# Kernel tuning notes

Hardware: AMD Instinct MI355X
Metric: run time of the kernel (lower is better)

Reference implementation:

```python
import jax, jax.numpy as jnp
import numpy as np

B, T, DM = 2, 512, 1024
H, DH = 16, 64          # n_heads, d_head = d_model // n_heads
D, R = 32, 4            # d_manifold, metric_net rank
TEMP_MIN = 0.5


def _rope_tables(t_len, d_head):
    inv_freq = 1.0 / (10000.0 ** (jnp.arange(0, d_head, 2, dtype=jnp.float32) / d_head))
    t = jnp.arange(t_len, dtype=jnp.float32)
    freqs = t[:, None] * inv_freq[None, :]          # [T, d_head//2]
    emb = jnp.concatenate([freqs, freqs], axis=-1)  # [T, d_head]
    return jnp.cos(emb), jnp.sin(emb)


def _apply_rope(x, cos, sin):
    # x: [B, H, T, d_head]
    half = x.shape[-1] // 2
    x1, x2 = x[..., :half], x[..., half:]
    c1 = cos[None, None, :, :half]
    s1 = sin[None, None, :, :half]
    return jnp.concatenate([x1 * c1 - x2 * s1, x1 * s1 + x2 * c1], axis=-1)


def setup_inputs() -> dict:
    key = jax.random.key(0)
    ks = jax.random.split(key, 9)
    s = 0.02
    return {
        "x": jax.random.normal(ks[0], (B, T, DM), dtype=jnp.float32),
        "Wq": s * jax.random.normal(ks[1], (DM, DM), dtype=jnp.float32),
        "Wk": s * jax.random.normal(ks[2], (DM, DM), dtype=jnp.float32),
        "Wv": s * jax.random.normal(ks[3], (DM, DM), dtype=jnp.float32),
        "Wo": s * jax.random.normal(ks[4], (DM, DM), dtype=jnp.float32),
        "Wqm": s * jax.random.normal(ks[5], (DH, D), dtype=jnp.float32),
        "Wkm": s * jax.random.normal(ks[6], (DH, D), dtype=jnp.float32),
        "Wmetric": s * jax.random.normal(ks[7], (D, D * R), dtype=jnp.float32),
        "temperature": jnp.asarray(1.0, dtype=jnp.float32),
    }


def reference(x, Wq, Wk, Wv, Wo, Wqm, Wkm, Wmetric, temperature):
    b, t, c = x.shape
    # projections -> [B, H, T, d_head]
    def split_heads(y):
        return y.reshape(b, t, H, DH).transpose(0, 2, 1, 3)
    q = split_heads(x @ Wq)
    k = split_heads(x @ Wk)
    v = split_heads(x @ Wv)

    cos, sin = _rope_tables(t, DH)
    q = _apply_rope(q, cos, sin)
    k = _apply_rope(k, cos, sin)

    # manifold coordinates in (0,1): [B, H, T, D]
    qm = jax.nn.sigmoid(jnp.einsum('bhtd,dm->bhtm', q, Wqm))
    km = jax.nn.sigmoid(jnp.einsum('bhtd,dm->bhtm', k, Wkm))

    # low-rank metric factor U(q): [B, H, T, D, R]
    U = jnp.einsum('bhtm,mn->bhtn', qm, Wmetric).reshape(b, H, t, D, R)

    # Euclidean part: ||q_i - k_j||^2 = |q|^2 + |k|^2 - 2 q.k  -> [B,H,T,T]
    q2 = jnp.sum(qm * qm, axis=-1)
    k2 = jnp.sum(km * km, axis=-1)
    qk = jnp.einsum('bhid,bhjd->bhij', qm, km)
    dist_euc = q2[..., :, None] + k2[..., None, :] - 2.0 * qk

    # low-rank part: ||U_i^T (q_i - k_j)||^2, factorized as U_i^T q_i - U_i^T k_j
    Uq = jnp.einsum('bhidr,bhid->bhir', U, qm)          # [B,H,T,R]
    Uk = jnp.einsum('bhidr,bhjd->bhijr', U, km)         # [B,H,T,T,R]
    dist_lr = jnp.sum((Uq[:, :, :, None, :] - Uk) ** 2, axis=-1)

    dist_sq = jnp.maximum(dist_euc + dist_lr, 0.0)

    temp = jnp.maximum(temperature, TEMP_MIN)
    attn = -dist_sq / temp

    causal = jnp.triu(jnp.ones((t, t), dtype=bool), k=1)
    attn = jnp.where(causal[None, None], -jnp.inf, attn)
    attn = jax.nn.softmax(attn, axis=-1)

    out = jnp.einsum('bhij,bhjd->bhid', attn, v)        # [B,H,T,d_head]
    out = out.transpose(0, 2, 1, 3).reshape(b, t, c)
    return out @ Wo
```

## Files before the change

### kernel.cpp

```cpp
#include <hip/hip_runtime.h>
#include <cmath>

constexpr int B_  = 2;
constexpr int T_  = 512;
constexpr int DM_ = 1024;
constexpr int H_  = 16;
constexpr int DH_ = 64;
constexpr int D_  = 32;
constexpr int R_  = 4;
constexpr int BH_ = B_ * H_;

typedef __bf16 bf16x8 __attribute__((ext_vector_type(8)));
typedef float  f32x4  __attribute__((ext_vector_type(4)));
typedef unsigned short u16x8 __attribute__((ext_vector_type(8)));

__device__ __forceinline__ unsigned short f2bf(float f) {
    unsigned u = __float_as_uint(f);
    return (unsigned short)((u + 0x7fffu + ((u >> 16) & 1u)) >> 16);
}
__device__ __forceinline__ float bf2f(unsigned short v) {
    return __uint_as_float((unsigned)v << 16);
}

__device__ __forceinline__ void gload16(const void* g, void* l) {
    __builtin_amdgcn_global_load_lds(
        (const __attribute__((address_space(1))) void*)g,
        (__attribute__((address_space(3))) void*)l, 16, 0, 0);
}

__global__ __launch_bounds__(256) void prep_kernel(
    const float* __restrict__ x,
    const float* __restrict__ Wq, const float* __restrict__ Wk,
    const float* __restrict__ Wv, const float* __restrict__ Wo,
    unsigned short* __restrict__ xb,
    unsigned short* __restrict__ wqb, unsigned short* __restrict__ wkb,
    unsigned short* __restrict__ wvb, unsigned short* __restrict__ wob)
{
    const int t = threadIdx.x;
    const int z = blockIdx.z;
    if (z == 4) {
        int base = (blockIdx.y * 16 + blockIdx.x) * 4096 + t * 16;
#pragma unroll
        for (int c = 0; c < 4; ++c) {
            float4 v = *(const float4*)&x[base + c * 4];
            ushort4 o = { f2bf(v.x), f2bf(v.y), f2bf(v.z), f2bf(v.w) };
            *(ushort4*)&xb[base + c * 4] = o;
        }
        return;
    }
    __shared__ __align__(16) unsigned short Ls[64][72];
    const float* W = (z == 0) ? Wq : (z == 1) ? Wk : (z == 2) ? Wv : Wo;
    unsigned short* O = (z == 0) ? wqb : (z == 1) ? wkb : (z == 2) ? wvb : wob;
    const int k0 = blockIdx.x * 64;
    const int n0 = blockIdx.y * 64;
#pragma unroll
    for (int it = 0; it < 4; ++it) {
        int r = it * 16 + (t >> 4);
        int c = (t & 15) * 4;
        float4 v4 = *(const float4*)&W[(size_t)(k0 + r) * DM_ + n0 + c];
        Ls[c + 0][r] = f2bf(v4.x); Ls[c + 1][r] = f2bf(v4.y);
        Ls[c + 2][r] = f2bf(v4.z); Ls[c + 3][r] = f2bf(v4.w);
    }
    __syncthreads();
#pragma unroll
    for (int it = 0; it < 2; ++it) {
        int nl = it * 32 + (t >> 3);
        int kc = (t & 7) * 8;
        *(u16x8*)&O[(size_t)(n0 + nl) * DM_ + k0 + kc] = *(const u16x8*)&Ls[nl][kc];
    }
}

template <int EPI>
__global__ __launch_bounds__(256) void mfma_gemm64(
    const unsigned short* __restrict__ A,
    const unsigned short* __restrict__ Bt0,
    const unsigned short* __restrict__ Bt1,
    const unsigned short* __restrict__ Bt2,
    float* __restrict__ C0, float* __restrict__ C1,
    unsigned short* __restrict__ vT)
{
    __shared__ __align__(16) unsigned short As[64 * 32];
    __shared__ __align__(16) unsigned short Bs[64 * 32];
    const int tid  = threadIdx.x;
    const int lane = tid & 63;
    const int w    = tid >> 6;
    const int wm   = (w & 1) * 32;
    const int wn   = (w >> 1) * 32;

    const int bm = blockIdx.y * 64;
    int bn, which = 0;
    const unsigned short* Bt;
    if (EPI == 0) {
        int n0 = blockIdx.x * 64;
        which = n0 >> 10;
        bn = n0 & 1023;
        Bt = (which == 0) ? Bt0 : (which == 1) ? Bt1 : Bt2;
    } else {
        bn = blockIdx.x * 64;
        Bt = Bt0;
    }

    f32x4 acc[2][2] = {};
    const int sr = tid >> 2;
    const int sc = (tid & 3) * 8;
    const unsigned short* Ap = A  + (size_t)(bm + sr) * DM_ + sc;
    const unsigned short* Bp = Bt + (size_t)(bn + sr) * DM_ + sc;
    unsigned short* AsP = &As[sr * 32 + sc];
    unsigned short* BsP = &Bs[sr * 32 + sc];
    const int fr = lane & 15;
    const int fq = (lane >> 4) * 8;

    for (int k0 = 0; k0 < DM_; k0 += 32) {
        gload16(Ap + k0, AsP);
        gload16(Bp + k0, BsP);
        __syncthreads();
        bf16x8 af[2], bfr[2];
#pragma unroll
        for (int i = 0; i < 2; ++i) {
            af[i]  = *(const bf16x8*)&As[(wm + i * 16 + fr) * 32 + fq];
            bfr[i] = *(const bf16x8*)&Bs[(wn + i * 16 + fr) * 32 + fq];
        }
#pragma unroll
        for (int mi = 0; mi < 2; ++mi)
#pragma unroll
            for (int ni = 0; ni < 2; ++ni)
                acc[mi][ni] = __builtin_amdgcn_mfma_f32_16x16x32_bf16(
                    af[mi], bfr[ni], acc[mi][ni], 0, 0, 0);
        __syncthreads();
    }

#pragma unroll
    for (int mi = 0; mi < 2; ++mi)
#pragma unroll
        for (int ni = 0; ni < 2; ++ni) {
            f32x4 a = acc[mi][ni];
            int col = bn + wn + ni * 16 + (lane & 15);
#pragma unroll
            for (int r = 0; r < 4; ++r) {
                int row = bm + wm + mi * 16 + (lane >> 4) * 4 + r;
                if (EPI == 0) {
                    int h = col >> 6, d = col & 63;
                    int bb = row >> 9, tt = row & (T_ - 1);
                    if (which == 2) {
                        vT[(((size_t)bb * H_ + h) * DH_ + d) * T_ + tt] = f2bf(a[r]);
                    } else {
                        float* C = (which == 0) ? C0 : C1;
                        C[(((size_t)bb * H_ + h) * T_ + tt) * DH_ + d] = a[r];
                    }
                } else {
                    C0[(size_t)row * DM_ + col] = a[r];
                }
            }
        }
}

__global__ __launch_bounds__(256) void feat_both(
    const float* __restrict__ q_raw, const float* __restrict__ k_raw,
    const float* __restrict__ Wqm,   const float* __restrict__ Wkm,
    const float* __restrict__ Wmetric,
    unsigned short* __restrict__ a_hi, unsigned short* __restrict__ a_lo,
    unsigned short* __restrict__ km_hi, unsigned short* __restrict__ km_lo,
    float* __restrict__ q2p, float* __restrict__ k2,
    unsigned short* __restrict__ Urb)
{
    const bool QSIDE = (blockIdx.y == 0);
    const float* raw = QSIDE ? q_raw : k_raw;
    const float* Wm  = QSIDE ? Wqm   : Wkm;

    __shared__ float qrs[4][64];
    __shared__ float qms[4][32];
    __shared__ float Us[4][128];
    __shared__ float Uqs[4][4];
    const int tid  = threadIdx.x;
    const int w    = tid >> 6;
    const int lane = tid & 63;
    const int row  = blockIdx.x * 4 + w;
    const int t    = row & (T_ - 1);
    const int bh   = row >> 9;

    float rv = raw[(size_t)row * 64 + lane];
    int   fi = lane & 31;
    float ang = (float)t * expf((float)fi * -0.28782313662425575f);
    float s, c;
    sincosf(ang, &s, &c);
    float partner = __shfl_xor(rv, 32);
    float qr = (lane < 32) ? (rv * c - partner * s) : (partner * s + rv * c);
    qrs[w][lane] = qr;
    __syncthreads();

    if (lane < 32) {
        float acc = 0.f;
#pragma unroll 8
        for (int d = 0; d < 64; ++d) acc += qrs[w][d] * Wm[d * 32 + lane];
        qms[w][lane] = 1.0f / (1.0f + __expf(-acc));
    }
    __syncthreads();

    if (QSIDE) {
        float a0 = 0.f, a1 = 0.f;
#pragma unroll 8
        for (int m = 0; m < 32; ++m) {
            float qv = qms[w][m];
            a0 += qv * Wmetric[m * 128 + lane];
            a1 += qv * Wmetric[m * 128 + 64 + lane];
        }
        Us[w][lane] = a0; Us[w][64 + lane] = a1;
        {
            int r0 = lane & 3, d0 = lane >> 2;
            int d1 = 16 + (lane >> 2);
            Urb[(((size_t)bh * R_ + r0) * T_ + t) * D_ + d0] = f2bf(a0);
            Urb[(((size_t)bh * R_ + r0) * T_ + t) * D_ + d1] = f2bf(a1);
        }
        __syncthreads();
        if (lane < 4) {
            float acc = 0.f;
#pragma unroll
            for (int d = 0; d < 32; ++d) acc += Us[w][d * 4 + lane] * qms[w][d];
            Uqs[w][lane] = acc;
        }
        __syncthreads();
        if (lane < 32) {
            float b = Uqs[w][0] * Us[w][lane * 4 + 0]
                    + Uqs[w][1] * Us[w][lane * 4 + 1]
                    + Uqs[w][2] * Us[w][lane * 4 + 2]
                    + Uqs[w][3] * Us[w][lane * 4 + 3];
            float a = qms[w][lane] + b;
            unsigned short hi = f2bf(a);
            unsigned short lo = f2bf(a - bf2f(hi));
            size_t off = (size_t)row * 32 + lane;
            a_hi[off] = hi; a_lo[off] = lo;
        }
        if (lane == 0) {
            float acc = 0.f;
#pragma unroll
            for (int m = 0; m < 32; ++m) acc += qms[w][m] * qms[w][m];
#pragma unroll
            for (int r = 0; r < 4; ++r) acc += Uqs[w][r] * Uqs[w][r];
            q2p[row] = acc;
        }
    } else {
        if (lane < 32) {
            float v = qms[w][lane];
            unsigned short hi = f2bf(v);
            unsigned short lo = f2bf(v - bf2f(hi));
            size_t off = (size_t)row * 32 + lane;
            km_hi[off] = hi; km_lo[off] = lo;
        }
        if (lane == 0) {
            float acc = 0.f;
#pragma unroll
            for (int m = 0; m < 32; ++m) acc += qms[w][m] * qms[w][m];
            k2[row] = acc;
        }
    }
}

constexpr int PROW = 40;
__global__ __launch_bounds__(256) void attn_mfma(
    const unsigned short* __restrict__ a_hi, const unsigned short* __restrict__ a_lo,
    const unsigned short* __restrict__ km_hi, const unsigned short* __restrict__ km_lo,
    const unsigned short* __restrict__ Urb,
    const float* __restrict__ q2p, const float* __restrict__ k2,
    const float* __restrict__ temp_p, const unsigned short* __restrict__ vT,
    unsigned short* __restrict__ ctxb)
{
    __shared__ __align__(16) unsigned short P_lds[4][32 * PROW];
    __shared__ __align__(16) float OP[4][32][64];
    __shared__ float ML[4][32];

    const int itile = blockIdx.x, bh = blockIdx.y;
    const int i0 = itile * 32;
    const int tid = threadIdx.x, w = tid >> 6, lane = tid & 63;
    const int l15 = lane & 15, quad = lane >> 4;

    const float inv_temp = 1.0f / fmaxf(temp_p[0], 0.5f);

    bf16x8 Ahi[2], Alo[2], Aur[4][2];
#pragma unroll
    for (int mi = 0; mi < 2; ++mi) {
        size_t ab = ((size_t)bh * T_ + i0 + mi * 16 + l15) * 32 + quad * 8;
        Ahi[mi] = *(const bf16x8*)&a_hi[ab];
        Alo[mi] = *(const bf16x8*)&a_lo[ab];
#pragma unroll
        for (int r = 0; r < 4; ++r)
            Aur[r][mi] = *(const bf16x8*)
                &Urb[(((size_t)bh * R_ + r) * T_ + i0 + mi * 16 + l15) * 32 + quad * 8];
    }
    float q2r[2][4];
#pragma unroll
    for (int mi = 0; mi < 2; ++mi)
#pragma unroll
        for (int rg = 0; rg < 4; ++rg)
            q2r[mi][rg] = q2p[(size_t)bh * T_ + i0 + mi * 16 + quad * 4 + rg];

    f32x4 Oacc[2][4] = {};
    float psum[2][4] = {};

    for (int jt = w; jt <= itile; jt += 4) {
        const int j0 = jt * 32;
        bf16x8 Bhi[2], Blo[2];
#pragma unroll
        for (int ni = 0; ni < 2; ++ni) {
            size_t kb = ((size_t)bh * T_ + j0 + ni * 16 + l15) * 32 + quad * 8;
            Bhi[ni] = *(const bf16x8*)&km_hi[kb];
            Blo[ni] = *(const bf16x8*)&km_lo[kb];
        }
        f32x4 acc[2][2] = {};
#pragma unroll
        for (int mi = 0; mi < 2; ++mi)
#pragma unroll
            for (int ni = 0; ni < 2; ++ni) {
                acc[mi][ni] = __builtin_amdgcn_mfma_f32_16x16x32_bf16(
                    Alo[mi], Bhi[ni], acc[mi][ni], 0, 0, 0);
                acc[mi][ni] = __builtin_amdgcn_mfma_f32_16x16x32_bf16(
                    Ahi[mi], Blo[ni], acc[mi][ni], 0, 0, 0);
                acc[mi][ni] = __builtin_amdgcn_mfma_f32_16x16x32_bf16(
                    Ahi[mi], Bhi[ni], acc[mi][ni], 0, 0, 0);
            }
        f32x4 sq[2][2] = {};
#pragma unroll
        for (int r = 0; r < 4; ++r) {
            f32x4 ar[2][2] = {};
#pragma unroll
            for (int mi = 0; mi < 2; ++mi)
#pragma unroll
                for (int ni = 0; ni < 2; ++ni)
                    ar[mi][ni] = __builtin_amdgcn_mfma_f32_16x16x32_bf16(
                        Aur[r][mi], Bhi[ni], ar[mi][ni], 0, 0, 0);
#pragma unroll
            for (int mi = 0; mi < 2; ++mi)
#pragma unroll
                for (int ni = 0; ni < 2; ++ni)
                    sq[mi][ni] += ar[mi][ni] * ar[mi][ni];
        }
        float k2c[2];
#pragma unroll
        for (int ni = 0; ni < 2; ++ni)
            k2c[ni] = k2[(size_t)bh * T_ + j0 + ni * 16 + l15];
        const bool diag = (jt == itile);
#pragma unroll
        for (int mi = 0; mi < 2; ++mi)
#pragma unroll
            for (int ni = 0; ni < 2; ++ni)
#pragma unroll
                for (int rg = 0; rg < 4; ++rg) {
                    float dist = q2r[mi][rg] + k2c[ni]
                               - 2.f * acc[mi][ni][rg] + sq[mi][ni][rg];
                    float sc = -fmaxf(dist, 0.f) * inv_temp;
                    if (diag && (ni * 16 + l15) > (mi * 16 + quad * 4 + rg))
                        sc = -1e30f;
                    float p = __expf(sc);
                    psum[mi][rg] += p;
                    P_lds[w][(mi * 16 + quad * 4 + rg) * PROW + ni * 16 + l15] = f2bf(p);
                }
        bf16x8 Pf[2], Vf[4];
#pragma unroll
        for (int mi = 0; mi < 2; ++mi)
            Pf[mi] = *(const bf16x8*)&P_lds[w][(mi * 16 + l15) * PROW + quad * 8];
#pragma unroll
        for (int n4 = 0; n4 < 4; ++n4)
            Vf[n4] = *(const bf16x8*)
                &vT[((size_t)bh * DH_ + n4 * 16 + l15) * T_ + j0 + quad * 8];
#pragma unroll
        for (int mi = 0; mi < 2; ++mi)
#pragma unroll
            for (int n4 = 0; n4 < 4; ++n4)
                Oacc[mi][n4] = __builtin_amdgcn_mfma_f32_16x16x32_bf16(
                    Pf[mi], Vf[n4], Oacc[mi][n4], 0, 0, 0);
    }

#pragma unroll
    for (int mi = 0; mi < 2; ++mi)
#pragma unroll
        for (int rg = 0; rg < 4; ++rg) {
            float v = psum[mi][rg];
            v += __shfl_xor(v, 1); v += __shfl_xor(v, 2);
            v += __shfl_xor(v, 4); v += __shfl_xor(v, 8);
            psum[mi][rg] = v;
        }
    if (l15 == 0)
#pragma unroll
        for (int mi = 0; mi < 2; ++mi)
#pragma unroll
            for (int rg = 0; rg < 4; ++rg)
                ML[w][mi * 16 + quad * 4 + rg] = psum[mi][rg];
#pragma unroll
    for (int mi = 0; mi < 2; ++mi)
#pragma unroll
        for (int n4 = 0; n4 < 4; ++n4)
#pragma unroll
            for (int rg = 0; rg < 4; ++rg)
                OP[w][mi * 16 + quad * 4 + rg][n4 * 16 + l15] = Oacc[mi][n4][rg];
    __syncthreads();

    const int ii = tid >> 3, ds = tid & 7;
    float l = ML[0][ii] + ML[1][ii] + ML[2][ii] + ML[3][ii];
    float O[8] = {};
#pragma unroll
    for (int wv = 0; wv < 4; ++wv) {
        float4 o0 = *(const float4*)&OP[wv][ii][ds * 8];
        float4 o1 = *(const float4*)&OP[wv][ii][ds * 8 + 4];
        O[0] += o0.x; O[1] += o0.y; O[2] += o0.z; O[3] += o0.w;
        O[4] += o1.x; O[5] += o1.y; O[6] += o1.z; O[7] += o1.w;
    }
    const float inv = 1.0f / l;
    const int b = bh >> 4, h = bh & 15;
    u16x8 o;
#pragma unroll
    for (int dd = 0; dd < 8; ++dd) o[dd] = f2bf(O[dd] * inv);
    *(u16x8*)&ctxb[((size_t)b * T_ + i0 + ii) * DM_ + h * 64 + ds * 8] = o;
}

extern "C" void kernel_launch(void* const* d_in, const int* in_sizes, int n_in,
                              void* d_out, int out_size, void* d_ws, size_t ws_size,
                              hipStream_t stream)
{
    const float* x       = (const float*)d_in[0];
    const float* Wq      = (const float*)d_in[1];
    const float* Wk      = (const float*)d_in[2];
    const float* Wv      = (const float*)d_in[3];
    const float* Wo      = (const float*)d_in[4];
    const float* Wqm     = (const float*)d_in[5];
    const float* Wkm     = (const float*)d_in[6];
    const float* Wmetric = (const float*)d_in[7];
    const float* temp    = (const float*)d_in[8];
    float* out = (float*)d_out;
    float* ws  = (float*)d_ws;

    float* q_raw = ws;
    float* k_raw = q_raw + (size_t)BH_ * T_ * DH_;
    float* q2p   = k_raw + (size_t)BH_ * T_ * DH_;
    float* k2    = q2p   + (size_t)BH_ * T_;
    unsigned short* xb    = (unsigned short*)(k2 + (size_t)BH_ * T_);
    unsigned short* wqb   = xb    + (size_t)DM_ * DM_;
    unsigned short* wkb   = wqb   + (size_t)DM_ * DM_;
    unsigned short* wvb   = wkb   + (size_t)DM_ * DM_;
    unsigned short* wob   = wvb   + (size_t)DM_ * DM_;
    unsigned short* a_hi  = wob   + (size_t)DM_ * DM_;
    unsigned short* a_lo  = a_hi  + (size_t)BH_ * T_ * D_;
    unsigned short* kmhi  = a_lo  + (size_t)BH_ * T_ * D_;
    unsigned short* kmlo  = kmhi  + (size_t)BH_ * T_ * D_;
    unsigned short* Urb   = kmlo  + (size_t)BH_ * T_ * D_;
    unsigned short* vT    = Urb   + (size_t)BH_ * R_ * T_ * D_;
    unsigned short* ctxb  = (unsigned short*)q_raw;

    prep_kernel<<<dim3(16, 16, 5), 256, 0, stream>>>(
        x, Wq, Wk, Wv, Wo, xb, wqb, wkb, wvb, wob);
    mfma_gemm64<0><<<dim3(48, 16), 256, 0, stream>>>(
        xb, wqb, wkb, wvb, q_raw, k_raw, vT);
    feat_both<<<dim3(BH_ * T_ / 4, 2), 256, 0, stream>>>(
        q_raw, k_raw, Wqm, Wkm, Wmetric,
        a_hi, a_lo, kmhi, kmlo, q2p, k2, Urb);
    attn_mfma<<<dim3(T_ / 32, BH_), 256, 0, stream>>>(
        a_hi, a_lo, kmhi, kmlo, Urb, q2p, k2, temp, vT, ctxb);
    mfma_gemm64<1><<<dim3(16, 16), 256, 0, stream>>>(
        ctxb, wob, nullptr, nullptr, out, nullptr, nullptr);
}
```

Before: 156.2 us.

## Fuse RoPE and manifold feature computation into QKV GEMM epilogue

```diff
diff --git a/kernel.cpp b/kernel.cpp
--- a/kernel.cpp
+++ b/kernel.cpp
@@ -70,14 +70,194 @@
     }
 }
 
-template <int EPI>
-__global__ __launch_bounds__(256) void mfma_gemm64(
+__global__ __launch_bounds__(256) void qkv_feat_gemm(
     const unsigned short* __restrict__ A,
-    const unsigned short* __restrict__ Bt0,
-    const unsigned short* __restrict__ Bt1,
-    const unsigned short* __restrict__ Bt2,
-    float* __restrict__ C0, float* __restrict__ C1,
-    unsigned short* __restrict__ vT)
+    const unsigned short* __restrict__ wqb, const unsigned short* __restrict__ wkb,
+    const unsigned short* __restrict__ wvb,
+    const float* __restrict__ Wqm, const float* __restrict__ Wkm,
+    const float* __restrict__ Wmetric,
+    unsigned short* __restrict__ a_hi, unsigned short* __restrict__ a_lo,
+    unsigned short* __restrict__ km_hi, unsigned short* __restrict__ km_lo,
+    float* __restrict__ q2p, float* __restrict__ k2,
+    unsigned short* __restrict__ Urb, unsigned short* __restrict__ vT)
+{
+    __shared__ union {
+        struct { __align__(16) unsigned short As[64 * 32];
+                 __align__(16) unsigned short Bs[64 * 32]; } g;
+        struct { float Ct[64][65]; float qm[64][33]; } f;
+    } sh;
+
+    const int tid  = threadIdx.x;
+    const int lane = tid & 63;
+    const int w    = tid >> 6;
+    const int wm   = (w & 1) * 32;
+    const int wn   = (w >> 1) * 32;
+    const int l15  = lane & 15, quad = lane >> 4;
+
+    const int bm = blockIdx.y * 64;
+    const int n0 = blockIdx.x * 64;
+    const int which = n0 >> 10;
+    const int bn = n0 & 1023;
+    const int h  = bn >> 6;
+    const unsigned short* Bt = (which == 0) ? wqb : (which == 1) ? wkb : wvb;
+
+    f32x4 acc[2][2] = {};
+    const int sr = tid >> 2;
+    const int sc = (tid & 3) * 8;
+    const unsigned short* Ap = A  + (size_t)(bm + sr) * DM_ + sc;
+    const unsigned short* Bp = Bt + (size_t)(bn + sr) * DM_ + sc;
+    unsigned short* AsP = &sh.g.As[sr * 32 + sc];
+    unsigned short* BsP = &sh.g.Bs[sr * 32 + sc];
+
+    for (int k0 = 0; k0 < DM_; k0 += 32) {
+        gload16(Ap + k0, AsP);
+        gload16(Bp + k0, BsP);
+        __syncthreads();
+        bf16x8 af[2], bfr[2];
+#pragma unroll
+        for (int i = 0; i < 2; ++i) {
+            af[i]  = *(const bf16x8*)&sh.g.As[(wm + i * 16 + l15) * 32 + quad * 8];
+            bfr[i] = *(const bf16x8*)&sh.g.Bs[(wn + i * 16 + l15) * 32 + quad * 8];
+        }
+#pragma unroll
+        for (int mi = 0; mi < 2; ++mi)
+#pragma unroll
+            for (int ni = 0; ni < 2; ++ni)
+                acc[mi][ni] = __builtin_amdgcn_mfma_f32_16x16x32_bf16(
+                    af[mi], bfr[ni], acc[mi][ni], 0, 0, 0);
+        __syncthreads();
+    }
+
+    if (which == 2) {
+#pragma unroll
+        for (int mi = 0; mi < 2; ++mi)
+#pragma unroll
+            for (int ni = 0; ni < 2; ++ni) {
+                f32x4 a = acc[mi][ni];
+                int d = wn + ni * 16 + l15;
+#pragma unroll
+                for (int r = 0; r < 4; ++r) {
+                    int m = bm + wm + mi * 16 + quad * 4 + r;
+                    int bb = m >> 9, tt = m & (T_ - 1);
+                    vT[(((size_t)bb * H_ + h) * DH_ + d) * T_ + tt] = f2bf(a[r]);
+                }
+            }
+        return;
+    }
+
+#pragma unroll
+    for (int mi = 0; mi < 2; ++mi)
+#pragma unroll
+        for (int ni = 0; ni < 2; ++ni) {
+            f32x4 a = acc[mi][ni];
+            int cl = wn + ni * 16 + l15;
+#pragma unroll
+            for (int r = 0; r < 4; ++r)
+                sh.f.Ct[wm + mi * 16 + quad * 4 + r][cl] = a[r];
+        }
+    __syncthreads();
+
+    for (int e = tid; e < 2048; e += 256) {
+        int row = e >> 5, d = e & 31;
+        int t = (bm + row) & (T_ - 1);
+        float ang = (float)t * expf((float)d * -0.28782313662425575f);
+        float s, c;
+        sincosf(ang, &s, &c);
+        float v1 = sh.f.Ct[row][d], v2 = sh.f.Ct[row][d + 32];
+        sh.f.Ct[row][d]      = v1 * c - v2 * s;
+        sh.f.Ct[row][d + 32] = v1 * s + v2 * c;
+    }
+    __syncthreads();
+
+    const float* Wm = (which == 0) ? Wqm : Wkm;
+    const int r  = tid >> 2, c = tid & 3, mg = c * 8;
+    float a8[8] = {};
+    for (int d = 0; d < 64; ++d) {
+        float qr = sh.f.Ct[r][d];
+        float4 w0 = *(const float4*)&Wm[d * 32 + mg];
+        float4 w1 = *(const float4*)&Wm[d * 32 + mg + 4];
+        a8[0] = fmaf(qr, w0.x, a8[0]); a8[1] = fmaf(qr, w0.y, a8[1]);
+        a8[2] = fmaf(qr, w0.z, a8[2]); a8[3] = fmaf(qr, w0.w, a8[3]);
+        a8[4] = fmaf(qr, w1.x, a8[4]); a8[5] = fmaf(qr, w1.y, a8[5]);
+        a8[6] = fmaf(qr, w1.z, a8[6]); a8[7] = fmaf(qr, w1.w, a8[7]);
+    }
+#pragma unroll
+    for (int j = 0; j < 8; ++j) a8[j] = 1.0f / (1.0f + __expf(-a8[j]));
+
+    const int m_ = bm + r;
+    const int b_ = m_ >> 9, t_ = m_ & (T_ - 1);
+    const int bh = b_ * H_ + h;
+    const size_t rowg = (size_t)bh * T_ + t_;
+
+    if (which == 1) {
+        u16x8 hi8, lo8;
+#pragma unroll
+        for (int j = 0; j < 8; ++j) {
+            unsigned short hv = f2bf(a8[j]);
+            hi8[j] = hv; lo8[j] = f2bf(a8[j] - bf2f(hv));
+        }
+        *(u16x8*)&km_hi[rowg * 32 + mg] = hi8;
+        *(u16x8*)&km_lo[rowg * 32 + mg] = lo8;
+        float p = 0.f;
+#pragma unroll
+        for (int j = 0; j < 8; ++j) p = fmaf(a8[j], a8[j], p);
+        p += __shfl_xor(p, 1); p += __shfl_xor(p, 2);
+        if (c == 0) k2[rowg] = p;
+        return;
+    }
+
+#pragma unroll
+    for (int j = 0; j < 8; ++j) sh.f.qm[r][mg + j] = a8[j];
+    __syncthreads();
+
+    const int nc = c * 32;
+    float U[32] = {};
+    for (int m = 0; m < 32; ++m) {
+        float qv = sh.f.qm[r][m];
+        const float* wrow = &Wmetric[m * 128 + nc];
+#pragma unroll
+        for (int n4 = 0; n4 < 8; ++n4) {
+            float4 wv = *(const float4*)&wrow[n4 * 4];
+            U[n4 * 4 + 0] = fmaf(qv, wv.x, U[n4 * 4 + 0]);
+            U[n4 * 4 + 1] = fmaf(qv, wv.y, U[n4 * 4 + 1]);
+            U[n4 * 4 + 2] = fmaf(qv, wv.z, U[n4 * 4 + 2]);
+            U[n4 * 4 + 3] = fmaf(qv, wv.w, U[n4 * 4 + 3]);
+        }
+    }
+    float uq[4] = {};
+#pragma unroll
+    for (int n = 0; n < 32; ++n) {
+        int nn = nc + n, d = nn >> 2, rr = nn & 3;
+        Urb[((size_t)(bh * R_ + rr) * T_ + t_) * D_ + d] = f2bf(U[n]);
+        uq[rr] = fmaf(U[n], sh.f.qm[r][d], uq[rr]);
+    }
+#pragma unroll
+    for (int rr = 0; rr < 4; ++rr) {
+        uq[rr] += __shfl_xor(uq[rr], 1);
+        uq[rr] += __shfl_xor(uq[rr], 2);
+    }
+    u16x8 hi8, lo8;
+    float p = 0.f;
+#pragma unroll
+    for (int j = 0; j < 8; ++j) {
+        float qmv = sh.f.qm[r][mg + j];
+        float av = qmv + uq[0] * U[j * 4 + 0] + uq[1] * U[j * 4 + 1]
+                       + uq[2] * U[j * 4 + 2] + uq[3] * U[j * 4 + 3];
+        unsigned short hv = f2bf(av);
+        hi8[j] = hv; lo8[j] = f2bf(av - bf2f(hv));
+        p = fmaf(qmv, qmv, p);
+    }
+    *(u16x8*)&a_hi[rowg * 32 + mg] = hi8;
+    *(u16x8*)&a_lo[rowg * 32 + mg] = lo8;
+    p += __shfl_xor(p, 1); p += __shfl_xor(p, 2);
+    if (c == 0)
+        q2p[rowg] = p + uq[0] * uq[0] + uq[1] * uq[1]
+                      + uq[2] * uq[2] + uq[3] * uq[3];
+}
+
+__global__ __launch_bounds__(256) void out_gemm64(
+    const unsigned short* __restrict__ A, const unsigned short* __restrict__ Bt,
+    float* __restrict__ C)
 {
     __shared__ __align__(16) unsigned short As[64 * 32];
     __shared__ __align__(16) unsigned short Bs[64 * 32];
@@ -86,19 +266,8 @@
     const int w    = tid >> 6;
     const int wm   = (w & 1) * 32;
     const int wn   = (w >> 1) * 32;
-
     const int bm = blockIdx.y * 64;
-    int bn, which = 0;
-    const unsigned short* Bt;
-    if (EPI == 0) {
-        int n0 = blockIdx.x * 64;
-        which = n0 >> 10;
-        bn = n0 & 1023;
-        Bt = (which == 0) ? Bt0 : (which == 1) ? Bt1 : Bt2;
-    } else {
-        bn = blockIdx.x * 64;
-        Bt = Bt0;
-    }
+    const int bn = blockIdx.x * 64;
 
     f32x4 acc[2][2] = {};
     const int sr = tid >> 2;
@@ -128,7 +297,6 @@
                     af[mi], bfr[ni], acc[mi][ni], 0, 0, 0);
         __syncthreads();
     }
-
 #pragma unroll
     for (int mi = 0; mi < 2; ++mi)
 #pragma unroll
@@ -138,121 +306,9 @@
 #pragma unroll
             for (int r = 0; r < 4; ++r) {
                 int row = bm + wm + mi * 16 + (lane >> 4) * 4 + r;
-                if (EPI == 0) {
-                    int h = col >> 6, d = col & 63;
-                    int bb = row >> 9, tt = row & (T_ - 1);
-                    if (which == 2) {
-                        vT[(((size_t)bb * H_ + h) * DH_ + d) * T_ + tt] = f2bf(a[r]);
-                    } else {
-                        float* C = (which == 0) ? C0 : C1;
-                        C[(((size_t)bb * H_ + h) * T_ + tt) * DH_ + d] = a[r];
-                    }
-                } else {
-                    C0[(size_t)row * DM_ + col] = a[r];
-                }
+                C[(size_t)row * DM_ + col] = a[r];
             }
         }
-}
-
-__global__ __launch_bounds__(256) void feat_both(
-    const float* __restrict__ q_raw, const float* __restrict__ k_raw,
-    const float* __restrict__ Wqm,   const float* __restrict__ Wkm,
-    const float* __restrict__ Wmetric,
-    unsigned short* __restrict__ a_hi, unsigned short* __restrict__ a_lo,
-    unsigned short* __restrict__ km_hi, unsigned short* __restrict__ km_lo,
-    float* __restrict__ q2p, float* __restrict__ k2,
-    unsigned short* __restrict__ Urb)
-{
-    const bool QSIDE = (blockIdx.y == 0);
-    const float* raw = QSIDE ? q_raw : k_raw;
-    const float* Wm  = QSIDE ? Wqm   : Wkm;
-
-    __shared__ float qrs[4][64];
-    __shared__ float qms[4][32];
-    __shared__ float Us[4][128];
-    __shared__ float Uqs[4][4];
-    const int tid  = threadIdx.x;
-    const int w    = tid >> 6;
-    const int lane = tid & 63;
-    const int row  = blockIdx.x * 4 + w;
-    const int t    = row & (T_ - 1);
-    const int bh   = row >> 9;
-
-    float rv = raw[(size_t)row * 64 + lane];
-    int   fi = lane & 31;
-    float ang = (float)t * expf((float)fi * -0.28782313662425575f);
-    float s, c;
-    sincosf(ang, &s, &c);
-    float partner = __shfl_xor(rv, 32);
-    float qr = (lane < 32) ? (rv * c - partner * s) : (partner * s + rv * c);
-    qrs[w][lane] = qr;
-    __syncthreads();
-
-    if (lane < 32) {
-        float acc = 0.f;
-#pragma unroll 8
-        for (int d = 0; d < 64; ++d) acc += qrs[w][d] * Wm[d * 32 + lane];
-        qms[w][lane] = 1.0f / (1.0f + __expf(-acc));
-    }
-    __syncthreads();
-
-    if (QSIDE) {
-        float a0 = 0.f, a1 = 0.f;
-#pragma unroll 8
-        for (int m = 0; m < 32; ++m) {
-            float qv = qms[w][m];
-            a0 += qv * Wmetric[m * 128 + lane];
-            a1 += qv * Wmetric[m * 128 + 64 + lane];
-        }
-        Us[w][lane] = a0; Us[w][64 + lane] = a1;
-        {
-            int r0 = lane & 3, d0 = lane >> 2;
-            int d1 = 16 + (lane >> 2);
-            Urb[(((size_t)bh * R_ + r0) * T_ + t) * D_ + d0] = f2bf(a0);
-            Urb[(((size_t)bh * R_ + r0) * T_ + t) * D_ + d1] = f2bf(a1);
-        }
-        __syncthreads();
-        if (lane < 4) {
-            float acc = 0.f;
-#pragma unroll
-            for (int d = 0; d < 32; ++d) acc += Us[w][d * 4 + lane] * qms[w][d];
-            Uqs[w][lane] = acc;
-        }
-        __syncthreads();
-        if (lane < 32) {
-            float b = Uqs[w][0] * Us[w][lane * 4 + 0]
-                    + Uqs[w][1] * Us[w][lane * 4 + 1]
-                    + Uqs[w][2] * Us[w][lane * 4 + 2]
-                    + Uqs[w][3] * Us[w][lane * 4 + 3];
-            float a = qms[w][lane] + b;
-            unsigned short hi = f2bf(a);
-            unsigned short lo = f2bf(a - bf2f(hi));
-            size_t off = (size_t)row * 32 + lane;
-            a_hi[off] = hi; a_lo[off] = lo;
-        }
-        if (lane == 0) {
-            float acc = 0.f;
-#pragma unroll
-            for (int m = 0; m < 32; ++m) acc += qms[w][m] * qms[w][m];
-#pragma unroll
-            for (int r = 0; r < 4; ++r) acc += Uqs[w][r] * Uqs[w][r];
-            q2p[row] = acc;
-        }
-    } else {
-        if (lane < 32) {
-            float v = qms[w][lane];
-            unsigned short hi = f2bf(v);
-            unsigned short lo = f2bf(v - bf2f(hi));
-            size_t off = (size_t)row * 32 + lane;
-            km_hi[off] = hi; km_lo[off] = lo;
-        }
-        if (lane == 0) {
-            float acc = 0.f;
-#pragma unroll
-            for (int m = 0; m < 32; ++m) acc += qms[w][m] * qms[w][m];
-            k2[row] = acc;
-        }
-    }
 }
 
 constexpr int PROW = 40;
@@ -427,32 +483,27 @@
     float* out = (float*)d_out;
     float* ws  = (float*)d_ws;
 
-    float* q_raw = ws;
-    float* k_raw = q_raw + (size_t)BH_ * T_ * DH_;
-    float* q2p   = k_raw + (size_t)BH_ * T_ * DH_;
-    float* k2    = q2p   + (size_t)BH_ * T_;
-    unsigned short* xb    = (unsigned short*)(k2 + (size_t)BH_ * T_);
-    unsigned short* wqb   = xb    + (size_t)DM_ * DM_;
-    unsigned short* wkb   = wqb   + (size_t)DM_ * DM_;
-    unsigned short* wvb   = wkb   + (size_t)DM_ * DM_;
-    unsigned short* wob   = wvb   + (size_t)DM_ * DM_;
-    unsigned short* a_hi  = wob   + (size_t)DM_ * DM_;
-    unsigned short* a_lo  = a_hi  + (size_t)BH_ * T_ * D_;
-    unsigned short* kmhi  = a_lo  + (size_t)BH_ * T_ * D_;
-    unsigned short* kmlo  = kmhi  + (size_t)BH_ * T_ * D_;
-    unsigned short* Urb   = kmlo  + (size_t)BH_ * T_ * D_;
-    unsigned short* vT    = Urb   + (size_t)BH_ * R_ * T_ * D_;
-    unsigned short* ctxb  = (unsigned short*)q_raw;
+    float* q2p = ws;
+    float* k2  = q2p + (size_t)BH_ * T_;
+    unsigned short* xb   = (unsigned short*)(k2 + (size_t)BH_ * T_);
+    unsigned short* wqb  = xb   + (size_t)DM_ * DM_;
+    unsigned short* wkb  = wqb  + (size_t)DM_ * DM_;
+    unsigned short* wvb  = wkb  + (size_t)DM_ * DM_;
+    unsigned short* wob  = wvb  + (size_t)DM_ * DM_;
+    unsigned short* a_hi = wob  + (size_t)DM_ * DM_;
+    unsigned short* a_lo = a_hi + (size_t)BH_ * T_ * D_;
+    unsigned short* kmhi = a_lo + (size_t)BH_ * T_ * D_;
+    unsigned short* kmlo = kmhi + (size_t)BH_ * T_ * D_;
+    unsigned short* Urb  = kmlo + (size_t)BH_ * T_ * D_;
+    unsigned short* vT   = Urb  + (size_t)BH_ * R_ * T_ * D_;
+    unsigned short* ctxb = vT   + (size_t)BH_ * DH_ * T_;
 
     prep_kernel<<<dim3(16, 16, 5), 256, 0, stream>>>(
         x, Wq, Wk, Wv, Wo, xb, wqb, wkb, wvb, wob);
-    mfma_gemm64<0><<<dim3(48, 16), 256, 0, stream>>>(
-        xb, wqb, wkb, wvb, q_raw, k_raw, vT);
-    feat_both<<<dim3(BH_ * T_ / 4, 2), 256, 0, stream>>>(
-        q_raw, k_raw, Wqm, Wkm, Wmetric,
-        a_hi, a_lo, kmhi, kmlo, q2p, k2, Urb);
+    qkv_feat_gemm<<<dim3(48, 16), 256, 0, stream>>>(
+        xb, wqb, wkb, wvb, Wqm, Wkm, Wmetric,
+        a_hi, a_lo, kmhi, kmlo, q2p, k2, Urb, vT);
     attn_mfma<<<dim3(T_ / 32, BH_), 256, 0, stream>>>(
         a_hi, a_lo, kmhi, kmlo, Urb, q2p, k2, temp, vT, ctxb);
-    mfma_gemm64<1><<<dim3(16, 16), 256, 0, stream>>>(
-        ctxb, wob, nullptr, nullptr, out, nullptr, nullptr);
-}
+    out_gemm64<<<dim3(16, 16), 256, 0, stream>>>(ctxb, wob, out);
+}
```

New measurement: 175.4 us. 12.3% more time.
